# Optimization experiments

Measured on AMD Instinct MI355X. Metric: run time of the kernel, lower is better.

## Reference

```python
import jax, jax.numpy as jnp
import numpy as np

HIDDEN = 1024
N_HEADS = 16
D_HEAD = HIDDEN // N_HEADS


def _rope(q, k):
    # q, k: [B, H, N, d]; interleaved-pair rotation as in the torch module
    B, H, N, d = q.shape
    inv_freq = 1.0 / (10000.0 ** (jnp.arange(0, d, 2, dtype=jnp.float32) / d))  # [d/2]
    pos = jnp.arange(N, dtype=jnp.float32)
    thetas = pos[:, None] * inv_freq[None, :]            # [N, d/2]
    cos, sin = jnp.cos(thetas), jnp.sin(thetas)

    def rot(x):
        xp = x.reshape(B, H, N, d // 2, 2)
        xx, xy = xp[..., 0], xp[..., 1]
        rx = xx * cos - xy * sin
        ry = xx * sin + xy * cos
        return jnp.stack([rx, ry], axis=-1).reshape(B, H, N, d)

    return rot(q), rot(k)


def setup_inputs() -> dict:
    key = jax.random.key(0)
    ks = jax.random.split(key, 9)
    B, N, Hd = 4, 2048, HIDDEN
    s = 1.0 / np.sqrt(Hd)
    return {
        "x": jax.random.normal(ks[0], (B, N, Hd), jnp.float32),
        "Wq": jax.random.normal(ks[1], (Hd, Hd), jnp.float32) * s,
        "bq": jax.random.normal(ks[2], (Hd,), jnp.float32) * 0.02,
        "Wk": jax.random.normal(ks[3], (Hd, Hd), jnp.float32) * s,
        "bk": jax.random.normal(ks[4], (Hd,), jnp.float32) * 0.02,
        "Wv": jax.random.normal(ks[5], (Hd, Hd), jnp.float32) * s,
        "bv": jax.random.normal(ks[6], (Hd,), jnp.float32) * 0.02,
        "Wo": jax.random.normal(ks[7], (Hd, Hd), jnp.float32) * s,
        "bo": jax.random.normal(ks[8], (Hd,), jnp.float32) * 0.02,
    }


def reference(x, Wq, bq, Wk, bk, Wv, bv, Wo, bo):
    B, N, _ = x.shape
    H, d = N_HEADS, D_HEAD
    # torch nn.Linear: y = x @ W.T + b
    q = (x @ Wq.T + bq).reshape(B, N, H, d).transpose(0, 2, 1, 3)  # [B,H,N,d]
    k = (x @ Wk.T + bk).reshape(B, N, H, d).transpose(0, 2, 1, 3)
    v = (x @ Wv.T + bv).reshape(B, N, H, d).transpose(0, 2, 1, 3)
    q, k = _rope(q, k)
    scores = jnp.einsum("bhnd,bhmd->bhnm", q, k) / jnp.sqrt(jnp.asarray(d, x.dtype))
    attn = jax.nn.softmax(scores, axis=-1)
    out = jnp.einsum("bhnm,bhmd->bhnd", attn, v)
    out = out.transpose(0, 2, 1, 3).reshape(B, N, H * d)
    return out @ Wo.T + bo
```

## Files before the change

### kernel.cpp

```cpp
#include <hip/hip_runtime.h>
#include <cmath>

typedef unsigned short u16;
typedef unsigned int u32;
typedef __bf16 bf16_t;
typedef bf16_t bf16x8 __attribute__((ext_vector_type(8)));
typedef float f32x4 __attribute__((ext_vector_type(4)));
typedef u32 u32x4 __attribute__((ext_vector_type(4)));

#define AS1 __attribute__((address_space(1)))
#define AS3 __attribute__((address_space(3)))

__device__ __forceinline__ void g2l16(const void* g, void* l) {
  __builtin_amdgcn_global_load_lds((const AS1 void*)g, (AS3 void*)l, 16, 0, 0);
}

__device__ __forceinline__ u16 f2b(float f) {
  u32 u = __builtin_bit_cast(u32, f);
  u += 0x7FFFu + ((u >> 16) & 1u);
  return (u16)(u >> 16);
}
__device__ __forceinline__ float b2f(u16 h) {
  u32 u = ((u32)h) << 16;
  return __builtin_bit_cast(float, u);
}

__device__ __forceinline__ float exp2fast(float x) {
#if __has_builtin(__builtin_amdgcn_exp2f)
  return __builtin_amdgcn_exp2f(x);
#else
  return exp2f(x);
#endif
}

__device__ __forceinline__ float sin01(float rev) {
#if __has_builtin(__builtin_amdgcn_sinf)
  return __builtin_amdgcn_sinf(rev);
#else
  return __sinf(rev * 6.283185307179586f);
#endif
}
__device__ __forceinline__ float cos01(float rev) {
#if __has_builtin(__builtin_amdgcn_cosf)
  return __builtin_amdgcn_cosf(rev);
#else
  return __cosf(rev * 6.283185307179586f);
#endif
}

__device__ __forceinline__ u32 cvtpk(float lo, float hi) {
  u32 d;
  asm("v_cvt_pk_bf16_f32 %0, %1, %2" : "=v"(d) : "v"(lo), "v"(hi));
  return d;
}

__global__ void mha_f2b_kernel(const float* __restrict__ in, u16* __restrict__ out, int n4) {
  int i = blockIdx.x * blockDim.x + threadIdx.x;
  if (i >= n4) return;
  float4 f = reinterpret_cast<const float4*>(in)[i];
  ushort4 o;
  o.x = f2b(f.x); o.y = f2b(f.y); o.z = f2b(f.z); o.w = f2b(f.w);
  reinterpret_cast<ushort4*>(out)[i] = o;
}

__global__ void mha_f2b4_kernel(const float* __restrict__ a0, const float* __restrict__ a1,
                                const float* __restrict__ a2, const float* __restrict__ a3,
                                u16* __restrict__ o0, u16* __restrict__ o1,
                                u16* __restrict__ o2, u16* __restrict__ o3, int n4) {
  int y = blockIdx.y;
  const float* in = y == 0 ? a0 : y == 1 ? a1 : y == 2 ? a2 : a3;
  u16* out = y == 0 ? o0 : y == 1 ? o1 : y == 2 ? o2 : o3;
  int i = blockIdx.x * blockDim.x + threadIdx.x;
  if (i >= n4) return;
  float4 f = reinterpret_cast<const float4*>(in)[i];
  ushort4 o;
  o.x = f2b(f.x); o.y = f2b(f.y); o.z = f2b(f.z); o.w = f2b(f.w);
  reinterpret_cast<ushort4*>(out)[i] = o;
}

#define BM 128
#define BN 128
#define BK 64

__global__ __launch_bounds__(256) void mha_gemm_bt(
    const u16* __restrict__ A, const u16* __restrict__ Bm,
    const float* __restrict__ bias,
    float* __restrict__ Cf,
    int M, int N, int K)
{
  __shared__ u16 As[BM * BK];
  __shared__ u16 Bs[BN * BK];
  const int tid = threadIdx.x;
  const int wid = tid >> 6, lane = tid & 63;
  const int r16 = lane & 15, g = lane >> 4;
  const int orig = blockIdx.x;
  const int lid = (orig & 7) * 64 + (orig >> 3);
  const int bm = (lid >> 3) * BM, bn = (lid & 7) * BN;
  const int wm = (wid >> 1) * 64, wn = (wid & 1) * 64;

  f32x4 acc[4][4] = {};

  const int sr = tid >> 3;
  const int sb = (tid & 7) * 16;

  for (int kt = 0; kt < K; kt += BK) {
#pragma unroll
    for (int p = 0; p < 4; ++p) {
      int ra = p * 32 + sr;
      int csw = (sb ^ ((ra & 7) << 4)) >> 1;
      g2l16(A  + (size_t)(bm + ra) * K + kt + csw, (u16*)As + p * 2048 + wid * 512);
      g2l16(Bm + (size_t)(bn + ra) * K + kt + csw, (u16*)Bs + p * 2048 + wid * 512);
    }
    __syncthreads();
#pragma unroll
    for (int c = 0; c < 2; ++c) {
      bf16x8 af[4], bfr[4];
#pragma unroll
      for (int mf = 0; mf < 4; ++mf) {
        int rr = wm + mf * 16 + r16;
        int ob = (c * 64 + g * 16) ^ ((rr & 7) << 4);
        af[mf] = *reinterpret_cast<const bf16x8*>(&As[rr * 64 + (ob >> 1)]);
      }
#pragma unroll
      for (int nf = 0; nf < 4; ++nf) {
        int rr = wn + nf * 16 + r16;
        int ob = (c * 64 + g * 16) ^ ((rr & 7) << 4);
        bfr[nf] = *reinterpret_cast<const bf16x8*>(&Bs[rr * 64 + (ob >> 1)]);
      }
      __builtin_amdgcn_s_setprio(1);
#pragma unroll
      for (int mf = 0; mf < 4; ++mf)
#pragma unroll
        for (int nf = 0; nf < 4; ++nf)
          acc[mf][nf] = __builtin_amdgcn_mfma_f32_16x16x32_bf16(af[mf], bfr[nf], acc[mf][nf], 0, 0, 0);
      __builtin_amdgcn_s_setprio(0);
    }
    __syncthreads();
  }

#pragma unroll
  for (int mf = 0; mf < 4; ++mf)
#pragma unroll
    for (int nf = 0; nf < 4; ++nf) {
      int col = bn + wn + nf * 16 + r16;
      float bv = bias[col];
#pragma unroll
      for (int r = 0; r < 4; ++r) {
        int rowm = bm + wm + mf * 16 + g * 4 + r;
        Cf[(size_t)rowm * N + col] = acc[mf][nf][r] + bv;
      }
    }
}

__global__ __launch_bounds__(256) void mha_gemm_qkv(
    const u16* __restrict__ A,
    const u16* __restrict__ W0, const u16* __restrict__ W1, const u16* __restrict__ W2,
    const float* __restrict__ b0, const float* __restrict__ b1, const float* __restrict__ b2,
    u16* __restrict__ C0, u16* __restrict__ C1, u16* __restrict__ Vt,
    int M, int N, int K)
{
  __shared__ u16 As[BM * BK];
  __shared__ u16 Bs[BN * BK];
  const int tid = threadIdx.x;
  const int wid = tid >> 6, lane = tid & 63;
  const int r16 = lane & 15, g = lane >> 4;
  const int orig = blockIdx.x;
  const int lid = (orig & 7) * 192 + (orig >> 3);
  const int wcol = lid % 24;
  const int wsel = wcol >> 3;
  const u16* Bm = wsel == 0 ? W0 : (wsel == 1 ? W1 : W2);
  const float* bias = wsel == 0 ? b0 : (wsel == 1 ? b1 : b2);
  const int bm = (lid / 24) * BM, bn = (wcol & 7) * BN;
  const int wm = (wid >> 1) * 64, wn = (wid & 1) * 64;

  f32x4 acc[4][4] = {};

  const int sr = tid >> 3;
  const int sb = (tid & 7) * 16;

  for (int kt = 0; kt < K; kt += BK) {
#pragma unroll
    for (int p = 0; p < 4; ++p) {
      int ra = p * 32 + sr;
      int csw = (sb ^ ((ra & 7) << 4)) >> 1;
      g2l16(A  + (size_t)(bm + ra) * K + kt + csw, (u16*)As + p * 2048 + wid * 512);
      g2l16(Bm + (size_t)(bn + ra) * K + kt + csw, (u16*)Bs + p * 2048 + wid * 512);
    }
    __syncthreads();
#pragma unroll
    for (int c = 0; c < 2; ++c) {
      bf16x8 af[4], bfr[4];
#pragma unroll
      for (int mf = 0; mf < 4; ++mf) {
        int rr = wm + mf * 16 + r16;
        int ob = (c * 64 + g * 16) ^ ((rr & 7) << 4);
        af[mf] = *reinterpret_cast<const bf16x8*>(&As[rr * 64 + (ob >> 1)]);
      }
#pragma unroll
      for (int nf = 0; nf < 4; ++nf) {
        int rr = wn + nf * 16 + r16;
        int ob = (c * 64 + g * 16) ^ ((rr & 7) << 4);
        bfr[nf] = *reinterpret_cast<const bf16x8*>(&Bs[rr * 64 + (ob >> 1)]);
      }
      __builtin_amdgcn_s_setprio(1);
#pragma unroll
      for (int mf = 0; mf < 4; ++mf)
#pragma unroll
        for (int nf = 0; nf < 4; ++nf)
          acc[mf][nf] = __builtin_amdgcn_mfma_f32_16x16x32_bf16(af[mf], bfr[nf], acc[mf][nf], 0, 0, 0);
      __builtin_amdgcn_s_setprio(0);
    }
    __syncthreads();
  }

  if (wsel == 2) {
#pragma unroll
    for (int mf = 0; mf < 4; ++mf) {
      int rowbase = bm + wm + mf * 16 + g * 4;
      int bb = rowbase >> 11;
      int nb = rowbase & 2047;
#pragma unroll
      for (int nf = 0; nf < 4; ++nf) {
        int col = bn + wn + nf * 16 + r16;
        float bv = bias[col];
        int hh = col >> 6, dd = col & 63;
        u16 w0 = f2b(acc[mf][nf][0] + bv);
        u16 w1 = f2b(acc[mf][nf][1] + bv);
        u16 w2 = f2b(acc[mf][nf][2] + bv);
        u16 w3 = f2b(acc[mf][nf][3] + bv);
        uint2 pkt;
        pkt.x = (u32)w0 | ((u32)w1 << 16);
        pkt.y = (u32)w2 | ((u32)w3 << 16);
        *reinterpret_cast<uint2*>(Vt + ((size_t)((bb * 16 + hh) * 64 + dd)) * 2048 + nb) = pkt;
      }
    }
  } else {
    u16* Cb = wsel == 0 ? C0 : C1;
    const float oscale = wsel == 0 ? 0.18033688011111793f : 1.0f;
#pragma unroll
    for (int nf = 0; nf < 4; ++nf) {
      int col = bn + wn + nf * 16 + r16;
      float bv = bias[col];
      int j = (nf * 16 + r16) >> 1;
      float invj = exp2f(-(float)j * 0.41524101186092503f);
      float invrev = invj * 0.15915494309189535f;
#pragma unroll
      for (int mf = 0; mf < 4; ++mf) {
#pragma unroll
        for (int r = 0; r < 4; ++r) {
          int rowm = bm + wm + mf * 16 + g * 4 + r;
          float v = acc[mf][nf][r] + bv;
          float pv = __shfl_xor(v, 1);
          float rev = (float)(rowm & 2047) * invrev;
          rev -= floorf(rev);
          float sn = sin01(rev), cs = cos01(rev);
          float tt = pv * sn;
          float res = fmaf(v, cs, (r16 & 1) ? tt : -tt);
          Cb[(size_t)rowm * N + col] = f2b(res * oscale);
        }
      }
    }
  }
}

#define QT 256
#define KVT 128
#define NKV 16

__global__ __launch_bounds__(512) void mha_attn_kernel(
    const u16* __restrict__ Q, const u16* __restrict__ Kmat,
    const u16* __restrict__ Vt, u16* __restrict__ Ao)
{
  __shared__ u16 Ks[2][KVT * 64];
  __shared__ u16 Vs[2][64 * KVT];
  const int tid = threadIdx.x;
  const int wid = tid >> 6, lane = tid & 63;
  const int r16 = lane & 15, g = lane >> 4;
  const int bh = blockIdx.x;
  const int b = bh >> 4, h = bh & 15;
  const int q0 = blockIdx.y * QT;
  const int wr = wid * 32;

  const u32x4 onesw = {0x3F803F80u, 0x3F803F80u, 0x3F803F80u, 0x3F803F80u};
  const bf16x8 onesf = __builtin_bit_cast(bf16x8, onesw);

  bf16x8 qf[2][2];
#pragma unroll
  for (int qb = 0; qb < 2; ++qb)
#pragma unroll
    for (int c = 0; c < 2; ++c)
      qf[qb][c] = *reinterpret_cast<const bf16x8*>(
          Q + (size_t)(b * 2048 + q0 + wr + qb * 16 + r16) * 1024 + h * 64 + c * 32 + g * 8);

  f32x4 accO[2][4] = {};
  f32x4 accL[2] = {};

  const int rk = tid >> 3, cbk = (tid & 7) * 16;
  const int rv = tid >> 4, cbv = (tid & 15) * 16;

  auto STAGE = [&](int buf, int j0) {
#pragma unroll
    for (int p = 0; p < 2; ++p) {
      int rr = p * 64 + rk;
      int csw = (cbk ^ ((rr & 7) << 4)) >> 1;
      g2l16(Kmat + (size_t)(b * 2048 + j0 + rr) * 1024 + h * 64 + csw,
            (u16*)Ks[buf] + p * 4096 + wid * 512);
    }
#pragma unroll
    for (int p = 0; p < 2; ++p) {
      int dd = p * 32 + rv;
      int csw = (cbv ^ ((dd & 7) << 4)) >> 1;
      g2l16(Vt + (size_t)(bh * 64 + dd) * 2048 + j0 + csw,
            (u16*)Vs[buf] + p * 4096 + wid * 512);
    }
  };

  STAGE(0, 0);
  __syncthreads();

  for (int t = 0; t < NKV; ++t) {
    const int cur = t & 1;
    if (t + 1 < NKV) STAGE(cur ^ 1, (t + 1) * KVT);

    f32x4 s[2][8] = {};
    const u16* KsC = Ks[cur];
#pragma unroll
    for (int c = 0; c < 2; ++c) {
      bf16x8 kf[8];
#pragma unroll
      for (int nf = 0; nf < 8; ++nf) {
        int rr = nf * 16 + r16;
        int ob = (c * 64 + g * 16) ^ ((rr & 7) << 4);
        kf[nf] = *reinterpret_cast<const bf16x8*>(&KsC[rr * 64 + (ob >> 1)]);
      }
      __builtin_amdgcn_s_setprio(1);
#pragma unroll
      for (int qb = 0; qb < 2; ++qb)
#pragma unroll
        for (int nf = 0; nf < 8; ++nf)
          s[qb][nf] = __builtin_amdgcn_mfma_f32_16x16x32_bf16(kf[nf], qf[qb][c], s[qb][nf], 0, 0, 0);
      __builtin_amdgcn_s_setprio(0);
    }

#pragma unroll
    for (int qb = 0; qb < 2; ++qb)
#pragma unroll
      for (int nf = 0; nf < 8; ++nf)
#pragma unroll
        for (int r = 0; r < 4; ++r)
          s[qb][nf][r] = exp2fast(s[qb][nf][r]);

    bf16x8 pa[2][4];
#pragma unroll
    for (int qb = 0; qb < 2; ++qb)
#pragma unroll
      for (int ks = 0; ks < 4; ++ks) {
        u32 X0 = cvtpk(s[qb][2 * ks][0], s[qb][2 * ks][1]);
        u32 X1 = cvtpk(s[qb][2 * ks][2], s[qb][2 * ks][3]);
        u32 Y0 = cvtpk(s[qb][2 * ks + 1][0], s[qb][2 * ks + 1][1]);
        u32 Y1 = cvtpk(s[qb][2 * ks + 1][2], s[qb][2 * ks + 1][3]);
        asm("v_permlane32_swap_b32 %0, %1" : "+v"(X0), "+v"(Y0));
        asm("v_permlane16_swap_b32 %0, %1" : "+v"(X0), "+v"(Y0));
        asm("v_permlane32_swap_b32 %0, %1" : "+v"(X1), "+v"(Y1));
        asm("v_permlane16_swap_b32 %0, %1" : "+v"(X1), "+v"(Y1));
        u32x4 w = {X0, X1, Y0, Y1};
        pa[qb][ks] = __builtin_bit_cast(bf16x8, w);
      }

    const u16* VsC = Vs[cur];
#pragma unroll
    for (int ks = 0; ks < 4; ++ks) {
      bf16x8 vb[4];
#pragma unroll
      for (int nf = 0; nf < 4; ++nf) {
        int dd = nf * 16 + r16;
        int ob = (ks * 64 + g * 16) ^ ((dd & 7) << 4);
        vb[nf] = *reinterpret_cast<const bf16x8*>(&VsC[dd * 128 + (ob >> 1)]);
      }
      __builtin_amdgcn_s_setprio(1);
#pragma unroll
      for (int qb = 0; qb < 2; ++qb) {
#pragma unroll
        for (int nf = 0; nf < 4; ++nf)
          accO[qb][nf] = __builtin_amdgcn_mfma_f32_16x16x32_bf16(pa[qb][ks], vb[nf], accO[qb][nf], 0, 0, 0);
        accL[qb] = __builtin_amdgcn_mfma_f32_16x16x32_bf16(pa[qb][ks], onesf, accL[qb], 0, 0, 0);
      }
      __builtin_amdgcn_s_setprio(0);
    }
    __syncthreads();
  }

#pragma unroll
  for (int qb = 0; qb < 2; ++qb) {
#pragma unroll
    for (int r = 0; r < 4; ++r) {
      float lb = 1.f / accL[qb][r];
      int rowm = q0 + wr + qb * 16 + g * 4 + r;
#pragma unroll
      for (int nf = 0; nf < 4; ++nf) {
        int dd = nf * 16 + r16;
        Ao[(size_t)(b * 2048 + rowm) * 1024 + h * 64 + dd] = f2b(accO[qb][nf][r] * lb);
      }
    }
  }
}

extern "C" void kernel_launch(void* const* d_in, const int* in_sizes, int n_in,
                              void* d_out, int out_size, void* d_ws, size_t ws_size,
                              hipStream_t stream)
{
  const float* x  = (const float*)d_in[0];
  const float* Wq = (const float*)d_in[1];
  const float* bq = (const float*)d_in[2];
  const float* Wk = (const float*)d_in[3];
  const float* bk = (const float*)d_in[4];
  const float* Wv = (const float*)d_in[5];
  const float* bv = (const float*)d_in[6];
  const float* Wo = (const float*)d_in[7];
  const float* bo = (const float*)d_in[8];
  float* out = (float*)d_out;

  char* ws = (char*)d_ws;
  u16* xb  = (u16*)(ws + 0);
  u16* Wqb = (u16*)(ws + 16777216);
  u16* Wkb = (u16*)(ws + 18874368);
  u16* Wvb = (u16*)(ws + 20971520);
  u16* Wob = (u16*)(ws + 23068672);
  u16* Qb  = (u16*)(ws + 25165824);
  u16* Kb  = (u16*)(ws + 41943040);
  u16* Vtb = (u16*)(ws + 58720256);
  u16* Ab  = (u16*)(ws + 75497472);

  mha_f2b_kernel<<<8192, 256, 0, stream>>>(x, xb, 2097152);
  mha_f2b4_kernel<<<dim3(1024, 4), 256, 0, stream>>>(Wq, Wk, Wv, Wo, Wqb, Wkb, Wvb, Wob, 262144);

  mha_gemm_qkv<<<1536, 256, 0, stream>>>(xb, Wqb, Wkb, Wvb, bq, bk, bv,
                                         Qb, Kb, Vtb, 8192, 1024, 1024);

  mha_attn_kernel<<<dim3(64, 8), 512, 0, stream>>>(Qb, Kb, Vtb, Ab);

  mha_gemm_bt<<<512, 256, 0, stream>>>(Ab, Wob, bo, out, 8192, 1024, 1024);
}
```

Before: 195.4 us.

## Drop LDS staging in attention; load K/V fragments directly from global

The attention kernel no longer double-buffers K and V tiles through shared memory. Each wave now loads its MFMA fragments straight from global memory (relying on L2/cache reuse across waves), which removes the barriers. The launch changes to 1024 blocks of 256 threads, and the block index is remapped so that blocks sharing a batch-head are spread across XCDs in groups. The risk is more global/L2 traffic and exposed load latency, since there is no software prefetch and no LDS reuse.

```diff
diff --git a/kernel.cpp b/kernel.cpp
--- a/kernel.cpp
+++ b/kernel.cpp
@@ -263,23 +263,21 @@
   }
 }
 
-#define QT 256
 #define KVT 128
 #define NKV 16
 
-__global__ __launch_bounds__(512) void mha_attn_kernel(
+__global__ __launch_bounds__(256) void mha_attn_kernel(
     const u16* __restrict__ Q, const u16* __restrict__ Kmat,
     const u16* __restrict__ Vt, u16* __restrict__ Ao)
 {
-  __shared__ u16 Ks[2][KVT * 64];
-  __shared__ u16 Vs[2][64 * KVT];
   const int tid = threadIdx.x;
   const int wid = tid >> 6, lane = tid & 63;
   const int r16 = lane & 15, g = lane >> 4;
-  const int bh = blockIdx.x;
+  const int orig = blockIdx.x;
+  const int lid = (orig & 7) * 128 + (orig >> 3);
+  const int bh = lid >> 4;
   const int b = bh >> 4, h = bh & 15;
-  const int q0 = blockIdx.y * QT;
-  const int wr = wid * 32;
+  const int q0 = (lid & 15) * 128 + wid * 32;
 
   const u32x4 onesw = {0x3F803F80u, 0x3F803F80u, 0x3F803F80u, 0x3F803F80u};
   const bf16x8 onesf = __builtin_bit_cast(bf16x8, onesw);
@@ -290,49 +288,25 @@
 #pragma unroll
     for (int c = 0; c < 2; ++c)
       qf[qb][c] = *reinterpret_cast<const bf16x8*>(
-          Q + (size_t)(b * 2048 + q0 + wr + qb * 16 + r16) * 1024 + h * 64 + c * 32 + g * 8);
+          Q + (size_t)(b * 2048 + q0 + qb * 16 + r16) * 1024 + h * 64 + c * 32 + g * 8);
 
   f32x4 accO[2][4] = {};
   f32x4 accL[2] = {};
 
-  const int rk = tid >> 3, cbk = (tid & 7) * 16;
-  const int rv = tid >> 4, cbv = (tid & 15) * 16;
-
-  auto STAGE = [&](int buf, int j0) {
-#pragma unroll
-    for (int p = 0; p < 2; ++p) {
-      int rr = p * 64 + rk;
-      int csw = (cbk ^ ((rr & 7) << 4)) >> 1;
-      g2l16(Kmat + (size_t)(b * 2048 + j0 + rr) * 1024 + h * 64 + csw,
-            (u16*)Ks[buf] + p * 4096 + wid * 512);
-    }
-#pragma unroll
-    for (int p = 0; p < 2; ++p) {
-      int dd = p * 32 + rv;
-      int csw = (cbv ^ ((dd & 7) << 4)) >> 1;
-      g2l16(Vt + (size_t)(bh * 64 + dd) * 2048 + j0 + csw,
-            (u16*)Vs[buf] + p * 4096 + wid * 512);
-    }
-  };
-
-  STAGE(0, 0);
-  __syncthreads();
+  const u16* Kbase = Kmat + (size_t)(b * 2048) * 1024 + h * 64;
+  const u16* Vbase = Vt + (size_t)(bh * 64) * 2048;
 
   for (int t = 0; t < NKV; ++t) {
-    const int cur = t & 1;
-    if (t + 1 < NKV) STAGE(cur ^ 1, (t + 1) * KVT);
+    const int j0 = t * KVT;
 
     f32x4 s[2][8] = {};
-    const u16* KsC = Ks[cur];
 #pragma unroll
     for (int c = 0; c < 2; ++c) {
       bf16x8 kf[8];
 #pragma unroll
-      for (int nf = 0; nf < 8; ++nf) {
-        int rr = nf * 16 + r16;
-        int ob = (c * 64 + g * 16) ^ ((rr & 7) << 4);
-        kf[nf] = *reinterpret_cast<const bf16x8*>(&KsC[rr * 64 + (ob >> 1)]);
-      }
+      for (int nf = 0; nf < 8; ++nf)
+        kf[nf] = *reinterpret_cast<const bf16x8*>(
+            Kbase + (size_t)(j0 + nf * 16 + r16) * 1024 + c * 32 + g * 8);
       __builtin_amdgcn_s_setprio(1);
 #pragma unroll
       for (int qb = 0; qb < 2; ++qb)
@@ -367,16 +341,13 @@
         pa[qb][ks] = __builtin_bit_cast(bf16x8, w);
       }
 
-    const u16* VsC = Vs[cur];
 #pragma unroll
     for (int ks = 0; ks < 4; ++ks) {
       bf16x8 vb[4];
 #pragma unroll
-      for (int nf = 0; nf < 4; ++nf) {
-        int dd = nf * 16 + r16;
-        int ob = (ks * 64 + g * 16) ^ ((dd & 7) << 4);
-        vb[nf] = *reinterpret_cast<const bf16x8*>(&VsC[dd * 128 + (ob >> 1)]);
-      }
+      for (int nf = 0; nf < 4; ++nf)
+        vb[nf] = *reinterpret_cast<const bf16x8*>(
+            Vbase + (size_t)(nf * 16 + r16) * 2048 + j0 + ks * 32 + g * 8);
       __builtin_amdgcn_s_setprio(1);
 #pragma unroll
       for (int qb = 0; qb < 2; ++qb) {
@@ -387,7 +358,6 @@
       }
       __builtin_amdgcn_s_setprio(0);
     }
-    __syncthreads();
   }
 
 #pragma unroll
@@ -395,7 +365,7 @@
 #pragma unroll
     for (int r = 0; r < 4; ++r) {
       float lb = 1.f / accL[qb][r];
-      int rowm = q0 + wr + qb * 16 + g * 4 + r;
+      int rowm = q0 + qb * 16 + g * 4 + r;
 #pragma unroll
       for (int nf = 0; nf < 4; ++nf) {
         int dd = nf * 16 + r16;
@@ -437,7 +407,7 @@
   mha_gemm_qkv<<<1536, 256, 0, stream>>>(xb, Wqb, Wkb, Wvb, bq, bk, bv,
                                          Qb, Kb, Vtb, 8192, 1024, 1024);
 
-  mha_attn_kernel<<<dim3(64, 8), 512, 0, stream>>>(Qb, Kb, Vtb, Ab);
+  mha_attn_kernel<<<1024, 256, 0, stream>>>(Qb, Kb, Vtb, Ab);
 
   mha_gemm_bt<<<512, 256, 0, stream>>>(Ab, Wob, bo, out, 8192, 1024, 1024);
 }
```

New measurement: 340.3 us. 1.74x slower.
